# Kernel tuning notes

Measured on AMD Instinct MI355X. Metric: run time of the kernel, lower is better.

## Reference

```python
import jax, jax.numpy as jnp
import numpy as np

HIDDEN = 2048
N_HEADS = 16
N_KV_HEADS = 4
HEAD_DIM = HIDDEN // N_HEADS  # 128
WINDOW = 1024
ROPE_THETA = 10000.0
B, S = 2, 2048


def setup_inputs() -> dict:
    key = jax.random.key(0)
    ks = jax.random.split(key, 8)
    gain = 2 ** (-2.5)
    def xavier(k, shape):
        fan_in, fan_out = shape
        lim = gain * np.sqrt(6.0 / (fan_in + fan_out))
        return jax.random.uniform(k, shape, jnp.float32, -lim, lim)
    kv_dim = N_KV_HEADS * HEAD_DIM
    return {
        "hidden_states": jax.random.normal(ks[0], (B, S, HIDDEN), jnp.float32),
        "position_ids": jnp.broadcast_to(jnp.arange(S, dtype=jnp.int64), (B, S)),
        "Wq": xavier(ks[1], (HIDDEN, HIDDEN)),  # [in, out]
        "bq": jnp.zeros((HIDDEN,), jnp.float32),
        "Wk": xavier(ks[2], (HIDDEN, kv_dim)),
        "bk": jnp.zeros((kv_dim,), jnp.float32),
        "Wv": xavier(ks[3], (HIDDEN, kv_dim)),
        "bv": jnp.zeros((kv_dim,), jnp.float32),
        "Wo": xavier(ks[4], (HIDDEN, HIDDEN)),
    }


def _rotate_half(x):
    x1, x2 = jnp.split(x, 2, axis=-1)
    return jnp.concatenate((-x2, x1), axis=-1)


def _rope_cos_sin(position_ids):
    # inv_freq: [head_dim/2]
    inv_freq = 1.0 / (ROPE_THETA ** (jnp.arange(0, HEAD_DIM, 2, dtype=jnp.float32) / HEAD_DIM))
    freqs = position_ids.astype(jnp.float32)[:, :, None] * inv_freq[None, None, :]  # [B,S,hd/2]
    emb = jnp.concatenate((freqs, freqs), axis=-1)  # [B,S,hd]
    return jnp.cos(emb), jnp.sin(emb)


def reference(hidden_states, position_ids, Wq, bq, Wk, bk, Wv, bv, Wo):
    b, s, _ = hidden_states.shape
    q = (hidden_states @ Wq + bq).reshape(b, s, N_HEADS, HEAD_DIM).transpose(0, 2, 1, 3)
    k = (hidden_states @ Wk + bk).reshape(b, s, N_KV_HEADS, HEAD_DIM).transpose(0, 2, 1, 3)
    v = (hidden_states @ Wv + bv).reshape(b, s, N_KV_HEADS, HEAD_DIM).transpose(0, 2, 1, 3)

    cos, sin = _rope_cos_sin(position_ids)  # [B,S,hd]
    cos, sin = cos[:, None], sin[:, None]   # unsqueeze head dim
    q = q * cos + _rotate_half(q) * sin
    k = k * cos + _rotate_half(k) * sin

    # GQA: repeat kv heads
    n_rep = N_HEADS // N_KV_HEADS
    k = jnp.repeat(k, n_rep, axis=1)
    v = jnp.repeat(v, n_rep, axis=1)

    # sliding-window causal mask (True = masked)
    k_pos = jnp.arange(s)
    q_abs = jnp.arange(s)  # K == Q (no cache)
    allowed = (k_pos[None, :] <= q_abs[:, None]) & (k_pos[None, :] > q_abs[:, None] - WINDOW)
    bias = jnp.where(allowed, 0.0, -jnp.inf).astype(q.dtype)  # [S,S]

    scale = 1.0 / np.sqrt(HEAD_DIM)
    scores = jnp.einsum("bhqd,bhkd->bhqk", q, k) * scale + bias[None, None]
    attn = jax.nn.softmax(scores, axis=-1)
    out = jnp.einsum("bhqk,bhkd->bhqd", attn, v)
    out = jnp.nan_to_num(out, nan=0.0)
    out = out.transpose(0, 2, 1, 3).reshape(b, s, N_HEADS * HEAD_DIM)
    return out @ Wo
```

## Files before the change

### kernel.cpp

```cpp
#include <hip/hip_runtime.h>
#include <hip/hip_bf16.h>

typedef __bf16 bf16_t;
typedef __bf16 bf16x8 __attribute__((ext_vector_type(8)));
typedef __bf16 bf16x4 __attribute__((ext_vector_type(4)));
typedef float  f32x4  __attribute__((ext_vector_type(4)));

#define HIDDEN 2048
#define NH     16
#define NKV    4
#define HD     128
#define WINDOW 1024
#define BB     2
#define SS     2048
#define ROWS   (BB*SS)
#define QKV_N  (HIDDEN + 2*NKV*HD)

#define AS1(p) ((const __attribute__((address_space(1))) void*)(p))
#define AS3(p) ((__attribute__((address_space(3))) void*)(p))


__global__ void k_convert_hs(const float* __restrict__ in, bf16_t* __restrict__ out) {
    int i = (blockIdx.x * 256 + threadIdx.x) * 4;
    float4 v = *(const float4*)(in + i);
    bf16x4 o;
    o[0] = (bf16_t)v.x; o[1] = (bf16_t)v.y; o[2] = (bf16_t)v.z; o[3] = (bf16_t)v.w;
    *(bf16x4*)(out + i) = o;
}

__global__ void k_transpose_w(const float* __restrict__ W, bf16_t* __restrict__ Wt,
                              int K, int N) {
    __shared__ float tile[32][33];
    int n0 = blockIdx.x * 32, k0 = blockIdx.y * 32;
    int tx = threadIdx.x & 31, ty = threadIdx.x >> 5;
    #pragma unroll
    for (int j = 0; j < 32; j += 8)
        tile[ty + j][tx] = W[(size_t)(k0 + ty + j) * N + n0 + tx];
    __syncthreads();
    #pragma unroll
    for (int j = 0; j < 32; j += 8)
        Wt[(size_t)(n0 + ty + j) * K + k0 + tx] = (bf16_t)tile[tx][ty + j];
}

__global__ void k_bias_concat(const float* __restrict__ bq, const float* __restrict__ bk,
                              const float* __restrict__ bv, float* __restrict__ out) {
    int i = blockIdx.x * 256 + threadIdx.x;
    if (i < HIDDEN)                 out[i] = bq[i];
    else if (i < HIDDEN + NKV*HD)   out[i] = bk[i - HIDDEN];
    else if (i < QKV_N)             out[i] = bv[i - HIDDEN - NKV*HD];
}

__global__ void k_rope_tab(float* __restrict__ tab) {
    int s = blockIdx.x, i = threadIdx.x;
    float freq = powf(10000.0f, -(float)i / 64.0f);
    float a = (float)s * freq;
    float sn, cs;
    sincosf(a, &sn, &cs);
    tab[s * 128 + i]      = cs;
    tab[s * 128 + 64 + i] = sn;
}


__global__ __launch_bounds__(512) void k_gemm256(
    const bf16_t* __restrict__ A, const bf16_t* __restrict__ Bt,
    const float* __restrict__ bias, float* __restrict__ C,
    int M, int N, int K)
{
    __shared__ bf16_t As[4][256 * 32];
    __shared__ bf16_t Bs[4][256 * 32];

    const int tid  = threadIdx.x;
    const int lane = tid & 63;
    const int wid  = tid >> 6;
    const int wm   = wid >> 2;
    const int wn   = wid & 3;
    const int l15  = lane & 15, lhi = lane >> 4;

    const int gx  = gridDim.x;
    const int nwg = gx * gridDim.y;
    const int id  = blockIdx.y * gx + blockIdx.x;
    const int cpx = nwg >> 3;
    const int swz = (id & 7) * cpx + (id >> 3);
    const int m0 = (swz / gx) * 256, n0 = (swz % gx) * 256;

    const int NT = K >> 5;

    const int r0_st = tid >> 2;
    const int j0_st = (tid & 3) ^ ((tid >> 3) & 3);
    const int r1_st = 128 + r0_st;
    const int j1_st = (tid & 3) ^ (((tid + 512) >> 3) & 3);

    auto STAGE = [&](int t, int buf) {
        const size_t kb = (size_t)t * 32;
        const char* gA0 = (const char*)(A  + (size_t)(m0 + r0_st) * K + kb) + j0_st*16;
        const char* gA1 = (const char*)(A  + (size_t)(m0 + r1_st) * K + kb) + j1_st*16;
        const char* gB0 = (const char*)(Bt + (size_t)(n0 + r0_st) * K + kb) + j0_st*16;
        const char* gB1 = (const char*)(Bt + (size_t)(n0 + r1_st) * K + kb) + j1_st*16;
        char* lA = (char*)As[buf] + tid * 16;
        char* lB = (char*)Bs[buf] + tid * 16;
        __builtin_amdgcn_global_load_lds(AS1(gA0), AS3(lA),        16, 0, 0);
        __builtin_amdgcn_global_load_lds(AS1(gA1), AS3(lA + 8192), 16, 0, 0);
        __builtin_amdgcn_global_load_lds(AS1(gB0), AS3(lB),        16, 0, 0);
        __builtin_amdgcn_global_load_lds(AS1(gB1), AS3(lB + 8192), 16, 0, 0);
    };

    const int rdoff = ((lhi ^ ((l15 >> 1) & 3)) << 4);

    f32x4 acc[8][4] = {};

    STAGE(0, 0); STAGE(1, 1); STAGE(2, 2);
    asm volatile("s_waitcnt vmcnt(8)" ::: "memory");
    __builtin_amdgcn_s_barrier();
    __builtin_amdgcn_sched_barrier(0);

    for (int t = 0; t < NT; ++t) {
        const int nb = t & 3;
        if (t + 3 < NT) STAGE(t + 3, (t + 3) & 3);

        const char* Ab = (const char*)As[nb] + (wm*128 + l15)*64 + rdoff;
        const char* Bb = (const char*)Bs[nb] + (wn*64  + l15)*64 + rdoff;
        bf16x8 af[8], bfv[4];
        #pragma unroll
        for (int mi = 0; mi < 8; ++mi)
            af[mi] = *(const bf16x8*)(Ab + mi*1024);
        #pragma unroll
        for (int ni = 0; ni < 4; ++ni)
            bfv[ni] = *(const bf16x8*)(Bb + ni*1024);

        __builtin_amdgcn_s_setprio(1);
        #pragma unroll
        for (int mi = 0; mi < 8; ++mi)
            #pragma unroll
            for (int ni = 0; ni < 4; ++ni)
                acc[mi][ni] = __builtin_amdgcn_mfma_f32_16x16x32_bf16(
                    af[mi], bfv[ni], acc[mi][ni], 0, 0, 0);
        __builtin_amdgcn_s_setprio(0);

        if (t + 3 < NT)      { asm volatile("s_waitcnt vmcnt(8)" ::: "memory"); }
        else if (t + 2 < NT) { asm volatile("s_waitcnt vmcnt(4)" ::: "memory"); }
        else if (t + 1 < NT) { asm volatile("s_waitcnt vmcnt(0)" ::: "memory"); }
        if (t + 1 < NT) {
            __builtin_amdgcn_s_barrier();
            __builtin_amdgcn_sched_barrier(0);
        }
    }

    #pragma unroll
    for (int mi = 0; mi < 8; ++mi) {
        #pragma unroll
        for (int ni = 0; ni < 4; ++ni) {
            int col = n0 + wn*64 + ni*16 + l15;
            float bv = bias ? bias[col] : 0.0f;
            #pragma unroll
            for (int r = 0; r < 4; ++r) {
                int row = m0 + wm*128 + mi*16 + lhi*4 + r;
                C[(size_t)row * N + col] = acc[mi][ni][r] + bv;
            }
        }
    }
}


__global__ void k_rope_scatter(const float* __restrict__ qkv, const float* __restrict__ tab,
                               bf16_t* __restrict__ Qr, bf16_t* __restrict__ Kr)
{
    const int row = blockIdx.x;
    const int b = row >> 11, s = row & (SS - 1);
    const float* base = qkv + (size_t)row * QKV_N;
    for (int p = threadIdx.x; p < (HIDDEN + NKV*HD) / 2; p += 256) {
        int head = p >> 6;
        int i = p & 63;
        float c  = tab[s*128 + i];
        float sn = tab[s*128 + 64 + i];
        float x1 = base[head*128 + i];
        float x2 = base[head*128 + 64 + i];
        float o1 = x1*c - x2*sn;
        float o2 = x2*c + x1*sn;
        if (head < NH) {
            bf16_t* o = Qr + ((size_t)((b*NH + head)*SS + s)) * HD;
            o[i] = (bf16_t)o1; o[64 + i] = (bf16_t)o2;
        } else {
            int kvh = head - NH;
            bf16_t* o = Kr + ((size_t)((b*NKV + kvh)*SS + s)) * HD;
            o[i] = (bf16_t)o1; o[64 + i] = (bf16_t)o2;
        }
    }
}


__global__ void k_v_transpose(const float* __restrict__ qkv, bf16_t* __restrict__ Vt)
{
    __shared__ bf16_t tile[64][HD + 8];
    const int bk = blockIdx.x;
    const int s0 = blockIdx.y * 64;
    const int b = bk >> 2, kvh = bk & 3;
    for (int li = threadIdx.x; li < 64 * HD; li += 256) {
        int i = li >> 7, d = li & 127;
        float v = qkv[(size_t)(b*SS + s0 + i) * QKV_N + HIDDEN + NKV*HD + kvh*HD + d];
        tile[i][d] = (bf16_t)v;
    }
    __syncthreads();
    for (int li = threadIdx.x; li < 64 * HD; li += 256) {
        int d = li >> 6, i = li & 63;
        Vt[((size_t)(b*NKV + kvh)*HD + d) * SS + s0 + i] = tile[i][d];
    }
}


__global__ __launch_bounds__(256) void k_attn(
    const bf16_t* __restrict__ Q, const bf16_t* __restrict__ Kk,
    const bf16_t* __restrict__ Vt, bf16_t* __restrict__ O)
{
    __shared__ bf16_t Ks[64 * 128];
    __shared__ bf16_t Vs[128 * 64];
    __shared__ bf16_t Plds[4][16][64];

    const int tid = threadIdx.x, lane = tid & 63, wid = tid >> 6;
    const int qt = 31 - (blockIdx.x >> 5);
    const int bh = blockIdx.x & 31;
    const int h  = bh & 15;
    const int b  = bh >> 4;
    const int q0 = qt * 64;
    const int kvh = h >> 2;
    const int l15 = lane & 15, lhi = lane >> 4;
    const float scale = 0.08838834764831845f;

    const bf16_t* Qp = Q + ((size_t)((b*NH + h)*SS + q0 + wid*16)) * HD;
    bf16x8 aq[4];
    #pragma unroll
    for (int ks = 0; ks < 4; ++ks)
        aq[ks] = *(const bf16x8*)(Qp + (size_t)l15 * HD + ks*32 + lhi*8);

    const char* Kg = (const char*)(Kk + (size_t)(b*NKV + kvh) * SS * HD);
    const char* Vg = (const char*)(Vt + (size_t)(b*NKV + kvh) * HD * SS);

    const int krow_st = tid >> 4;
    const int kcb_st  = (tid & 15) * 16;
    const int vrow_st = tid >> 3;
    const int vcb_st  = (tid & 7) * 16;

    f32x4 o_acc[8] = {};
    float m_run[4], l_run[4];
    #pragma unroll
    for (int r = 0; r < 4; ++r) { m_run[r] = -1e30f; l_run[r] = 0.0f; }

    int lo_j = q0 - (WINDOW - 1); if (lo_j < 0) lo_j = 0;
    const int kt_lo = lo_j >> 6;

    for (int kt = kt_lo; kt <= qt; ++kt) {
        const int k0 = kt * 64;

        #pragma unroll
        for (int j = 0; j < 4; ++j) {
            int krow = j*16 + krow_st;
            int ksrc = (k0 + krow) * 256 + (kcb_st ^ ((krow & 7) << 4));
            __builtin_amdgcn_global_load_lds(AS1(Kg + ksrc),
                AS3((char*)Ks + j*4096 + tid*16), 16, 0, 0);
            int vrow = j*32 + vrow_st;
            int vsrc = vrow * (SS*2) + k0*2 + (vcb_st ^ ((vrow & 7) << 4));
            __builtin_amdgcn_global_load_lds(AS1(Vg + vsrc),
                AS3((char*)Vs + j*4096 + tid*16), 16, 0, 0);
        }
        __syncthreads();

        f32x4 s_acc[4] = {};
        #pragma unroll
        for (int ni = 0; ni < 4; ++ni) {
            const int krow = ni*16 + l15;
            const char* kbase = (const char*)Ks + krow*256;
            const int sw = (krow & 7) << 4;
            #pragma unroll
            for (int ks = 0; ks < 4; ++ks) {
                bf16x8 bk = *(const bf16x8*)(kbase + ((ks*64 + lhi*16) ^ sw));
                s_acc[ni] = __builtin_amdgcn_mfma_f32_16x16x32_bf16(aq[ks], bk, s_acc[ni], 0, 0, 0);
            }
        }

        const bool full = (k0 + 63 <= q0) && (k0 >= q0 - 960);
        #pragma unroll
        for (int ni = 0; ni < 4; ++ni) {
            #pragma unroll
            for (int r = 0; r < 4; ++r) {
                float sv = s_acc[ni][r] * scale;
                if (!full) {
                    int key  = k0 + ni*16 + l15;
                    int qrow = q0 + wid*16 + lhi*4 + r;
                    bool ok = (key <= qrow) && (key > qrow - WINDOW);
                    sv = ok ? sv : -1e30f;
                }
                s_acc[ni][r] = sv;
            }
        }

        float rm[4];
        #pragma unroll
        for (int r = 0; r < 4; ++r)
            rm[r] = fmaxf(fmaxf(s_acc[0][r], s_acc[1][r]), fmaxf(s_acc[2][r], s_acc[3][r]));
        #pragma unroll
        for (int m = 1; m <= 8; m <<= 1)
            #pragma unroll
            for (int r = 0; r < 4; ++r)
                rm[r] = fmaxf(rm[r], __shfl_xor(rm[r], m, 64));

        float corr[4], rs[4];
        #pragma unroll
        for (int r = 0; r < 4; ++r) {
            float mnew = fmaxf(m_run[r], rm[r]);
            corr[r] = __expf(m_run[r] - mnew);
            m_run[r] = mnew;
            rs[r] = 0.0f;
        }
        #pragma unroll
        for (int ni = 0; ni < 4; ++ni) {
            #pragma unroll
            for (int r = 0; r < 4; ++r) {
                float sv = s_acc[ni][r];
                float p = (sv <= -1e29f) ? 0.0f : __expf(sv - m_run[r]);
                rs[r] += p;
                Plds[wid][lhi*4 + r][ni*16 + l15] = (bf16_t)p;
            }
        }
        #pragma unroll
        for (int m = 1; m <= 8; m <<= 1)
            #pragma unroll
            for (int r = 0; r < 4; ++r)
                rs[r] += __shfl_xor(rs[r], m, 64);
        #pragma unroll
        for (int r = 0; r < 4; ++r)
            l_run[r] = l_run[r] * corr[r] + rs[r];
        #pragma unroll
        for (int nj = 0; nj < 8; ++nj)
            #pragma unroll
            for (int r = 0; r < 4; ++r)
                o_acc[nj][r] *= corr[r];

        bf16x8 pa[2];
        #pragma unroll
        for (int ks2 = 0; ks2 < 2; ++ks2)
            pa[ks2] = *(const bf16x8*)(&Plds[wid][l15][ks2*32 + lhi*8]);
        #pragma unroll
        for (int nj = 0; nj < 8; ++nj) {
            const int vrow = nj*16 + l15;
            const char* vbase = (const char*)Vs + vrow*128;
            const int sw = (vrow & 7) << 4;
            #pragma unroll
            for (int ks2 = 0; ks2 < 2; ++ks2) {
                bf16x8 bv = *(const bf16x8*)(vbase + ((ks2*64 + lhi*16) ^ sw));
                o_acc[nj] = __builtin_amdgcn_mfma_f32_16x16x32_bf16(pa[ks2], bv, o_acc[nj], 0, 0, 0);
            }
        }
        __syncthreads();
    }

    #pragma unroll
    for (int r = 0; r < 4; ++r) {
        int qrow = q0 + wid*16 + lhi*4 + r;
        float inv = 1.0f / l_run[r];
        #pragma unroll
        for (int nj = 0; nj < 8; ++nj)
            O[(size_t)(b*SS + qrow) * HIDDEN + h*HD + nj*16 + l15] =
                (bf16_t)(o_acc[nj][r] * inv);
    }
}


extern "C" void kernel_launch(void* const* d_in, const int* in_sizes, int n_in,
                              void* d_out, int out_size, void* d_ws, size_t ws_size,
                              hipStream_t stream)
{
    const float* hs = (const float*)d_in[0];
    const float* Wq = (const float*)d_in[2];
    const float* bq = (const float*)d_in[3];
    const float* Wk = (const float*)d_in[4];
    const float* bk = (const float*)d_in[5];
    const float* Wv = (const float*)d_in[6];
    const float* bv = (const float*)d_in[7];
    const float* Wo = (const float*)d_in[8];
    float* out = (float*)d_out;

    char* ws = (char*)d_ws;
    size_t off = 0;
    auto alloc = [&](size_t bytes) {
        char* p = ws + off;
        off += (bytes + 255) & ~(size_t)255;
        return p;
    };
    bf16_t* hs_b   = (bf16_t*)alloc((size_t)ROWS * HIDDEN * 2);
    bf16_t* wqkv_t = (bf16_t*)alloc((size_t)QKV_N * HIDDEN * 2);
    bf16_t* wo_t   = (bf16_t*)alloc((size_t)HIDDEN * HIDDEN * 2);
    float*  biasc  = (float*) alloc((size_t)QKV_N * 4);
    float*  tab    = (float*) alloc((size_t)SS * 128 * 4);
    float*  qkv    = (float*) alloc((size_t)ROWS * QKV_N * 4);
    bf16_t* Qr     = (bf16_t*)alloc((size_t)BB * NH  * SS * HD * 2);
    bf16_t* Kr     = (bf16_t*)alloc((size_t)BB * NKV * SS * HD * 2);
    bf16_t* Vt     = (bf16_t*)alloc((size_t)BB * NKV * HD * SS * 2);
    bf16_t* attn_o = hs_b;

    k_convert_hs<<<(ROWS * HIDDEN) / 1024, 256, 0, stream>>>(hs, hs_b);
    k_transpose_w<<<dim3(HIDDEN/32, HIDDEN/32), 256, 0, stream>>>(Wq, wqkv_t, HIDDEN, HIDDEN);
    k_transpose_w<<<dim3((NKV*HD)/32, HIDDEN/32), 256, 0, stream>>>(
        Wk, wqkv_t + (size_t)HIDDEN * HIDDEN, HIDDEN, NKV*HD);
    k_transpose_w<<<dim3((NKV*HD)/32, HIDDEN/32), 256, 0, stream>>>(
        Wv, wqkv_t + (size_t)(HIDDEN + NKV*HD) * HIDDEN, HIDDEN, NKV*HD);
    k_transpose_w<<<dim3(HIDDEN/32, HIDDEN/32), 256, 0, stream>>>(Wo, wo_t, HIDDEN, HIDDEN);
    k_bias_concat<<<(QKV_N + 255) / 256, 256, 0, stream>>>(bq, bk, bv, biasc);
    k_rope_tab<<<SS, 64, 0, stream>>>(tab);

    k_gemm256<<<dim3(QKV_N/256, ROWS/256), 512, 0, stream>>>(
        hs_b, wqkv_t, biasc, qkv, ROWS, QKV_N, HIDDEN);
    k_rope_scatter<<<ROWS, 256, 0, stream>>>(qkv, tab, Qr, Kr);
    k_v_transpose<<<dim3(BB*NKV, SS/64), 256, 0, stream>>>(qkv, Vt);
    k_attn<<<BB * NH * (SS/64), 256, 0, stream>>>(Qr, Kr, Vt, attn_o);
    k_gemm256<<<dim3(HIDDEN/256, ROWS/256), 512, 0, stream>>>(
        attn_o, wo_t, nullptr, out, ROWS, HIDDEN, HIDDEN);
}
```

Baseline: 390.4 us.

## Template GEMM on M-tile, use 128-row tiles for output projection, split MFMA phases

Turns the GEMM into a template over the M tile height and launches the output projection with 128-row tiles, doubling its workgroup count from 128 to 256 so more CUs are filled. The inner loop is also split into two halves, each with its own LDS fragment load and workgroup barrier, so LDS reads and MFMAs interleave across waves. The vmcnt waits are adjusted for the smaller A staging. The extra barriers per k-step add sync overhead, and the smaller tile reduces B reuse.

```diff
diff --git a/kernel.cpp b/kernel.cpp
--- a/kernel.cpp
+++ b/kernel.cpp
@@ -61,12 +61,14 @@
 }
 
 
-__global__ __launch_bounds__(512) void k_gemm256(
+template <int BM>
+__global__ __launch_bounds__(512) void k_gemm(
     const bf16_t* __restrict__ A, const bf16_t* __restrict__ Bt,
     const float* __restrict__ bias, float* __restrict__ C,
     int M, int N, int K)
 {
-    __shared__ bf16_t As[4][256 * 32];
+    constexpr int MF = BM / 32;
+    __shared__ bf16_t As[4][BM * 32];
     __shared__ bf16_t Bs[4][256 * 32];
 
     const int tid  = threadIdx.x;
@@ -81,7 +83,7 @@
     const int id  = blockIdx.y * gx + blockIdx.x;
     const int cpx = nwg >> 3;
     const int swz = (id & 7) * cpx + (id >> 3);
-    const int m0 = (swz / gx) * 256, n0 = (swz % gx) * 256;
+    const int m0 = (swz / gx) * BM, n0 = (swz % gx) * 256;
 
     const int NT = K >> 5;
 
@@ -93,23 +95,34 @@
     auto STAGE = [&](int t, int buf) {
         const size_t kb = (size_t)t * 32;
         const char* gA0 = (const char*)(A  + (size_t)(m0 + r0_st) * K + kb) + j0_st*16;
-        const char* gA1 = (const char*)(A  + (size_t)(m0 + r1_st) * K + kb) + j1_st*16;
         const char* gB0 = (const char*)(Bt + (size_t)(n0 + r0_st) * K + kb) + j0_st*16;
         const char* gB1 = (const char*)(Bt + (size_t)(n0 + r1_st) * K + kb) + j1_st*16;
         char* lA = (char*)As[buf] + tid * 16;
         char* lB = (char*)Bs[buf] + tid * 16;
-        __builtin_amdgcn_global_load_lds(AS1(gA0), AS3(lA),        16, 0, 0);
-        __builtin_amdgcn_global_load_lds(AS1(gA1), AS3(lA + 8192), 16, 0, 0);
-        __builtin_amdgcn_global_load_lds(AS1(gB0), AS3(lB),        16, 0, 0);
+        __builtin_amdgcn_global_load_lds(AS1(gA0), AS3(lA), 16, 0, 0);
+        if constexpr (BM == 256) {
+            const char* gA1 = (const char*)(A + (size_t)(m0 + r1_st) * K + kb) + j1_st*16;
+            __builtin_amdgcn_global_load_lds(AS1(gA1), AS3(lA + 8192), 16, 0, 0);
+        }
+        __builtin_amdgcn_global_load_lds(AS1(gB0), AS3(lB), 16, 0, 0);
         __builtin_amdgcn_global_load_lds(AS1(gB1), AS3(lB + 8192), 16, 0, 0);
     };
 
+    auto WAIT2 = [&] {
+        if constexpr (BM == 256) asm volatile("s_waitcnt vmcnt(8)" ::: "memory");
+        else                     asm volatile("s_waitcnt vmcnt(6)" ::: "memory");
+    };
+    auto WAIT1 = [&] {
+        if constexpr (BM == 256) asm volatile("s_waitcnt vmcnt(4)" ::: "memory");
+        else                     asm volatile("s_waitcnt vmcnt(3)" ::: "memory");
+    };
+
     const int rdoff = ((lhi ^ ((l15 >> 1) & 3)) << 4);
 
-    f32x4 acc[8][4] = {};
+    f32x4 acc[MF][4] = {};
 
     STAGE(0, 0); STAGE(1, 1); STAGE(2, 2);
-    asm volatile("s_waitcnt vmcnt(8)" ::: "memory");
+    WAIT2();
     __builtin_amdgcn_s_barrier();
     __builtin_amdgcn_sched_barrier(0);
 
@@ -117,28 +130,46 @@
         const int nb = t & 3;
         if (t + 3 < NT) STAGE(t + 3, (t + 3) & 3);
 
-        const char* Ab = (const char*)As[nb] + (wm*128 + l15)*64 + rdoff;
-        const char* Bb = (const char*)Bs[nb] + (wn*64  + l15)*64 + rdoff;
-        bf16x8 af[8], bfv[4];
-        #pragma unroll
-        for (int mi = 0; mi < 8; ++mi)
+        const char* Ab = (const char*)As[nb] + (wm*(BM/2) + l15)*64 + rdoff;
+        const char* Bb = (const char*)Bs[nb] + (wn*64    + l15)*64 + rdoff;
+        bf16x8 af[MF], bfv[4];
+
+        #pragma unroll
+        for (int mi = 0; mi < MF/2; ++mi)
             af[mi] = *(const bf16x8*)(Ab + mi*1024);
         #pragma unroll
         for (int ni = 0; ni < 4; ++ni)
             bfv[ni] = *(const bf16x8*)(Bb + ni*1024);
-
+        __builtin_amdgcn_sched_barrier(0);
+        __builtin_amdgcn_s_barrier();
+        __builtin_amdgcn_sched_barrier(0);
         __builtin_amdgcn_s_setprio(1);
         #pragma unroll
-        for (int mi = 0; mi < 8; ++mi)
+        for (int mi = 0; mi < MF/2; ++mi)
             #pragma unroll
             for (int ni = 0; ni < 4; ++ni)
                 acc[mi][ni] = __builtin_amdgcn_mfma_f32_16x16x32_bf16(
                     af[mi], bfv[ni], acc[mi][ni], 0, 0, 0);
         __builtin_amdgcn_s_setprio(0);
 
-        if (t + 3 < NT)      { asm volatile("s_waitcnt vmcnt(8)" ::: "memory"); }
-        else if (t + 2 < NT) { asm volatile("s_waitcnt vmcnt(4)" ::: "memory"); }
-        else if (t + 1 < NT) { asm volatile("s_waitcnt vmcnt(0)" ::: "memory"); }
+        #pragma unroll
+        for (int mi = MF/2; mi < MF; ++mi)
+            af[mi] = *(const bf16x8*)(Ab + mi*1024);
+        __builtin_amdgcn_sched_barrier(0);
+        __builtin_amdgcn_s_barrier();
+        __builtin_amdgcn_sched_barrier(0);
+        __builtin_amdgcn_s_setprio(1);
+        #pragma unroll
+        for (int mi = MF/2; mi < MF; ++mi)
+            #pragma unroll
+            for (int ni = 0; ni < 4; ++ni)
+                acc[mi][ni] = __builtin_amdgcn_mfma_f32_16x16x32_bf16(
+                    af[mi], bfv[ni], acc[mi][ni], 0, 0, 0);
+        __builtin_amdgcn_s_setprio(0);
+
+        if (t + 3 < NT)      WAIT2();
+        else if (t + 2 < NT) WAIT1();
+        else if (t + 1 < NT) asm volatile("s_waitcnt vmcnt(0)" ::: "memory");
         if (t + 1 < NT) {
             __builtin_amdgcn_s_barrier();
             __builtin_amdgcn_sched_barrier(0);
@@ -146,14 +177,14 @@
     }
 
     #pragma unroll
-    for (int mi = 0; mi < 8; ++mi) {
+    for (int mi = 0; mi < MF; ++mi) {
         #pragma unroll
         for (int ni = 0; ni < 4; ++ni) {
             int col = n0 + wn*64 + ni*16 + l15;
             float bv = bias ? bias[col] : 0.0f;
             #pragma unroll
             for (int r = 0; r < 4; ++r) {
-                int row = m0 + wm*128 + mi*16 + lhi*4 + r;
+                int row = m0 + wm*(BM/2) + mi*16 + lhi*4 + r;
                 C[(size_t)row * N + col] = acc[mi][ni][r] + bv;
             }
         }
@@ -406,11 +437,11 @@
     k_bias_concat<<<(QKV_N + 255) / 256, 256, 0, stream>>>(bq, bk, bv, biasc);
     k_rope_tab<<<SS, 64, 0, stream>>>(tab);
 
-    k_gemm256<<<dim3(QKV_N/256, ROWS/256), 512, 0, stream>>>(
+    k_gemm<256><<<dim3(QKV_N/256, ROWS/256), 512, 0, stream>>>(
         hs_b, wqkv_t, biasc, qkv, ROWS, QKV_N, HIDDEN);
     k_rope_scatter<<<ROWS, 256, 0, stream>>>(qkv, tab, Qr, Kr);
     k_v_transpose<<<dim3(BB*NKV, SS/64), 256, 0, stream>>>(qkv, Vt);
     k_attn<<<BB * NH * (SS/64), 256, 0, stream>>>(Qr, Kr, Vt, attn_o);
-    k_gemm256<<<dim3(HIDDEN/256, ROWS/256), 512, 0, stream>>>(
+    k_gemm<128><<<dim3(HIDDEN/256, ROWS/128), 512, 0, stream>>>(
         attn_o, wo_t, nullptr, out, ROWS, HIDDEN, HIDDEN);
 }
```

After: 377.0 us. -3.4%, faster.
